# Performance work log

Hardware: AMD Instinct MI355X
Metric: run time of the kernel (lower is better)

Reference implementation:

```python
import jax, jax.numpy as jnp
import numpy as np

N_NODES = 100000


def _sage_conv(x, edge_index, W_l, W_r, b):
    # PyG SAGEConv (aggr='mean', root_weight=True, bias in lin_l):
    # out_i = W_l @ mean_{j in N(i)} x_j + b + W_r @ x_i
    src = edge_index[0]
    dst = edge_index[1]
    msg = x[src]                                              # [E, d] gather
    agg = jax.ops.segment_sum(msg, dst, num_segments=N_NODES)  # [N, d]
    deg = jax.ops.segment_sum(jnp.ones((src.shape[0],), x.dtype), dst,
                              num_segments=N_NODES)            # [N]
    agg = agg / jnp.maximum(deg, 1.0)[:, None]                 # mean, 0 if isolated
    return agg @ W_l.T + b + x @ W_r.T


def setup_inputs() -> dict:
    key = jax.random.key(0)
    ks = jax.random.split(key, 10)
    E, P = 1600000, 200000
    d_in, d_hid, d_out = 64, 128, 64
    s = 0.05
    return {
        "x": jax.random.normal(ks[0], (N_NODES, d_in), jnp.float32),
        "edge_index": jax.random.randint(ks[1], (2, E), 0, N_NODES, jnp.int32).astype(jnp.int64),
        "pairs": jax.random.randint(ks[2], (P, 2), 0, N_NODES, jnp.int32).astype(jnp.int64),
        "W1l": jax.random.normal(ks[3], (d_hid, d_in), jnp.float32) * s,
        "W1r": jax.random.normal(ks[4], (d_hid, d_in), jnp.float32) * s,
        "b1": jnp.zeros((d_hid,), jnp.float32),
        "W2l": jax.random.normal(ks[5], (d_out, d_hid), jnp.float32) * s,
        "W2r": jax.random.normal(ks[6], (d_out, d_hid), jnp.float32) * s,
        "b2": jnp.zeros((d_out,), jnp.float32),
        "Wlp": jax.random.normal(ks[7], (1, 2 * d_out), jnp.float32) * s,
        "blp": jnp.zeros((1,), jnp.float32),
    }


def reference(x, edge_index, pairs, W1l, W1r, b1, W2l, W2r, b2, Wlp, blp):
    h = _sage_conv(x, edge_index, W1l, W1r, b1)
    h = jax.nn.relu(h)
    h = _sage_conv(h, edge_index, W2l, W2r, b2)          # [N, d_out]
    src_emb = h[pairs[:, 0]]                              # [P, d_out]
    dst_emb = h[pairs[:, 1]]                              # [P, d_out]
    edge_emb = jnp.concatenate([src_emb, dst_emb], axis=1)  # [P, 2*d_out]
    logits = edge_emb @ Wlp.T + blp                       # [P, 1]
    return jax.nn.sigmoid(logits).squeeze(-1)             # [P]
```

## Files before the change

kernel.cpp:

```cpp
#include <hip/hip_runtime.h>


typedef __attribute__((ext_vector_type(8))) short bf16x8;
typedef __attribute__((ext_vector_type(4))) float f32x4;

#define NBLK_A 256

__device__ __forceinline__ unsigned short f2bf(float f) {
    unsigned u = __float_as_uint(f);
    u = u + 0x7fffu + ((u >> 16) & 1u);
    return (unsigned short)(u >> 16);
}
__device__ __forceinline__ float b2f(unsigned short s) {
    return __uint_as_float(((unsigned)s) << 16);
}
__device__ __forceinline__ float uflo(unsigned v) { return __uint_as_float(v << 16); }
__device__ __forceinline__ float ufhi(unsigned v) { return __uint_as_float(v & 0xffff0000u); }

__device__ __forceinline__ long load_idx(const void* p, long i, int is64) {
    if (is64) return (long)((const long long*)p)[i];
    return (long)((const int*)p)[i];
}

__device__ __forceinline__ int detect64_local(const void* p) {
    const unsigned* u = (const unsigned*)p;
    unsigned a = 0;
#pragma unroll
    for (int i = 0; i < 32; ++i) a |= u[2 * i + 1];
    return a == 0u;
}

__global__ void pre_kernel(const void* eidx, const float* __restrict__ x,
                           const float* __restrict__ W1l, const float* __restrict__ W1r,
                           const float* __restrict__ W2l, const float* __restrict__ W2r,
                           const float* __restrict__ b2, const float* __restrict__ Wlp,
                           const float* __restrict__ blp,
                           int* __restrict__ blk_hist, unsigned short* __restrict__ xa,
                           unsigned short* __restrict__ w1bf, float* __restrict__ wv,
                           int* __restrict__ flag,
                           long N, long E, int NBK, int chunk, int xcb) {
    int b = blockIdx.x;
    int tid = threadIdx.x;
    if (b < NBLK_A) {
        __shared__ int h[512];
        for (int i = tid; i < NBK; i += 256) h[i] = 0;
        __syncthreads();
        int is64 = detect64_local(eidx);
        long e0 = (long)b * chunk;
        long e1 = e0 + chunk; if (e1 > E) e1 = E;
        for (long e = e0 + tid; e < e1; e += 256) {
            long dst = load_idx(eidx, E + e, is64);
            atomicAdd(&h[(int)(dst >> 8)], 1);
        }
        __syncthreads();
        for (int i = tid; i < NBK; i += 256) blk_hist[i * NBLK_A + b] = h[i];
    } else if (b < NBLK_A + xcb) {
        long t = (long)(b - NBLK_A) * 256 + tid;
        long n = t >> 4;
        int q = (int)(t & 15);
        if (n >= N) return;
        float4 v = *(const float4*)&x[n * 64 + q * 4];
        uint2 u;
        u.x = (unsigned)f2bf(v.x) | ((unsigned)f2bf(v.y) << 16);
        u.y = (unsigned)f2bf(v.z) | ((unsigned)f2bf(v.w) << 16);
        *(uint2*)&xa[n * 128 + 64 + q * 4] = u;
    } else {
        if (tid == 0) *flag = detect64_local(eidx);
        if (tid < 128) {
            int k = tid;
            float s0 = 0.f, s1 = 0.f, s2 = 0.f, s3 = 0.f;
            for (int o = 0; o < 64; ++o) {
                float wl = Wlp[o], wr = Wlp[64 + o];
                float l = W2l[o * 128 + k], r = W2r[o * 128 + k];
                s0 += wl * l; s1 += wr * l; s2 += wl * r; s3 += wr * r;
            }
            wv[k] = s0; wv[128 + k] = s1; wv[256 + k] = s2; wv[384 + k] = s3;
            if (k == 0) {
                float c = blp[0];
                for (int o = 0; o < 64; ++o) c += (Wlp[o] + Wlp[64 + o]) * b2[o];
                wv[512] = c;
            }
        }
        for (int i = tid; i < 16384; i += 256) {
            int o = i >> 7, k = i & 127;
            float f = (k < 64) ? W1l[o * 64 + k] : W1r[o * 64 + (k - 64)];
            w1bf[i ^ ((o & 7) << 3)] = f2bf(f);
        }
    }
}

__global__ void bucket_total_kernel(const int* __restrict__ blk_hist, int* __restrict__ total) {
    __shared__ int ts[256];
    int k = blockIdx.x, t = threadIdx.x;
    ts[t] = blk_hist[k * NBLK_A + t];
    __syncthreads();
    for (int off = 128; off > 0; off >>= 1) {
        if (t < off) ts[t] += ts[t + off];
        __syncthreads();
    }
    if (t == 0) total[k] = ts[0];
}

__global__ void bucket_base_kernel(const int* __restrict__ total, int* __restrict__ base,
                                   int* __restrict__ row_start, int NBK, long N, long E) {
    int acc = 0;
    for (int k = 0; k < NBK; ++k) { base[k] = acc; acc += total[k]; }
    base[NBK] = acc;
    row_start[N] = (int)E;
}

__global__ void bucket_off_kernel(int* __restrict__ blk_hist, const int* __restrict__ base) {
    __shared__ int ts[256];
    int k = blockIdx.x, t = threadIdx.x;
    int v = blk_hist[k * NBLK_A + t];
    ts[t] = v; __syncthreads();
    for (int off = 1; off < 256; off <<= 1) {
        int u = (t >= off) ? ts[t - off] : 0;
        __syncthreads();
        ts[t] += u;
        __syncthreads();
    }
    blk_hist[k * NBLK_A + t] = base[k] + ts[t] - v;
}

__global__ void bucket_scatter_kernel(const void* eidx, const int* flag,
                                      const int* __restrict__ blk_hist,
                                      unsigned* __restrict__ ebuf, long E, int NBK, int chunk) {
    __shared__ int cur[512];
    int tid = threadIdx.x, b = blockIdx.x;
    for (int i = tid; i < NBK; i += 256) cur[i] = blk_hist[i * NBLK_A + b];
    __syncthreads();
    int is64 = *flag;
    long e0 = (long)b * chunk;
    long e1 = e0 + chunk; if (e1 > E) e1 = E;
    for (long e = e0 + tid; e < e1; e += 256) {
        long src = load_idx(eidx, e, is64);
        long dst = load_idx(eidx, E + e, is64);
        int pos = atomicAdd(&cur[(int)(dst >> 8)], 1);
        ebuf[pos] = (unsigned)src | ((unsigned)(dst & 255) << 24);
    }
}

__global__ void bucket_csr_kernel(const unsigned* __restrict__ ebuf, const int* __restrict__ base,
                                  int* __restrict__ csr_src, int* __restrict__ row_start, long N) {
    __shared__ int cnt[256], sc[256], cur[256];
    int k = blockIdx.x, t = threadIdx.x;
    int bstart = base[k], bend = base[k + 1];
    cnt[t] = 0;
    __syncthreads();
    for (int i = bstart + t; i < bend; i += 256)
        atomicAdd(&cnt[ebuf[i] >> 24], 1);
    __syncthreads();
    int c = cnt[t];
    sc[t] = c; __syncthreads();
    for (int off = 1; off < 256; off <<= 1) {
        int u = (t >= off) ? sc[t - off] : 0;
        __syncthreads();
        sc[t] += u;
        __syncthreads();
    }
    int loff = sc[t] - c;
    cur[t] = loff;
    long n = (long)k * 256 + t;
    if (n < N) row_start[n] = bstart + loff;
    __syncthreads();
    for (int i = bstart + t; i < bend; i += 256) {
        unsigned v = ebuf[i];
        int dl = (int)(v >> 24);
        int p = atomicAdd(&cur[dl], 1);
        csr_src[bstart + p] = (int)(v & 0xFFFFFFu);
    }
}

__global__ void gather_kernel(const int* __restrict__ rs, const int* __restrict__ csr,
                              const unsigned short* __restrict__ T,
                              unsigned short* __restrict__ Out, long N) {
    long gid = (long)blockIdx.x * 256 + threadIdx.x;
    long n = gid >> 6;
    if (n >= N) return;
    int lane = (int)(gid & 63);
    int lg = lane >> 4;
    int fq = lane & 15;
    int s = rs[n], e = rs[n + 1];
    unsigned boff = 64u + (unsigned)fq * 4u;
    float a0 = 0.f, a1 = 0.f, a2 = 0.f, a3 = 0.f;
    int j = s;
    for (; j + 16 <= e; j += 16) {
        unsigned o0 = ((unsigned)csr[j + lg] << 7) | boff;
        unsigned o1 = ((unsigned)csr[j + 4 + lg] << 7) | boff;
        unsigned o2 = ((unsigned)csr[j + 8 + lg] << 7) | boff;
        unsigned o3 = ((unsigned)csr[j + 12 + lg] << 7) | boff;
        uint2 r0 = *(const uint2*)&T[o0];
        uint2 r1 = *(const uint2*)&T[o1];
        uint2 r2 = *(const uint2*)&T[o2];
        uint2 r3 = *(const uint2*)&T[o3];
        a0 += uflo(r0.x); a1 += ufhi(r0.x); a2 += uflo(r0.y); a3 += ufhi(r0.y);
        a0 += uflo(r1.x); a1 += ufhi(r1.x); a2 += uflo(r1.y); a3 += ufhi(r1.y);
        a0 += uflo(r2.x); a1 += ufhi(r2.x); a2 += uflo(r2.y); a3 += ufhi(r2.y);
        a0 += uflo(r3.x); a1 += ufhi(r3.x); a2 += uflo(r3.y); a3 += ufhi(r3.y);
    }
    if (j < e) {
#pragma unroll
        for (int t = 0; t < 4; ++t) {
            int pos = j + 4 * t + lg;
            int ok = pos < e;
            unsigned oo = ((unsigned)csr[ok ? pos : s] << 7) | boff;
            uint2 r = *(const uint2*)&T[oo];
            float m = ok ? 1.f : 0.f;
            a0 += m * uflo(r.x); a1 += m * ufhi(r.x);
            a2 += m * uflo(r.y); a3 += m * ufhi(r.y);
        }
    }
    a0 += __shfl_xor(a0, 16, 64);  a1 += __shfl_xor(a1, 16, 64);
    a2 += __shfl_xor(a2, 16, 64);  a3 += __shfl_xor(a3, 16, 64);
    a0 += __shfl_xor(a0, 32, 64);  a1 += __shfl_xor(a1, 32, 64);
    a2 += __shfl_xor(a2, 32, 64);  a3 += __shfl_xor(a3, 32, 64);
    if (lg == 0) {
        float inv = 1.0f / fmaxf((float)(e - s), 1.0f);
        uint2 o;
        o.x = (unsigned)f2bf(a0 * inv) | ((unsigned)f2bf(a1 * inv) << 16);
        o.y = (unsigned)f2bf(a2 * inv) | ((unsigned)f2bf(a3 * inv) << 16);
        *(uint2*)&Out[((unsigned)n << 7) | ((unsigned)fq * 4u)] = o;
    }
}

__global__ __launch_bounds__(512) void fused_gemm_kernel(
        const unsigned short* __restrict__ A,
        const unsigned short* __restrict__ w1bf, const float* __restrict__ b1,
        const float* __restrict__ wv,
        float* __restrict__ ab, float* __restrict__ cd, long N) {
    __shared__ __align__(16) unsigned short wbuf[128 * 128];
    __shared__ __align__(16) unsigned short h1t[8][16 * 128];
    __shared__ float bs1[128];
    __shared__ float wvs[512];
    int tid = threadIdx.x;

    {
        const uint4* src = (const uint4*)w1bf;
        uint4* dst = (uint4*)wbuf;
#pragma unroll
        for (int i = 0; i < 4; ++i) dst[tid + i * 512] = src[tid + i * 512];
    }
    if (tid < 128) bs1[tid] = b1[tid];
    wvs[tid] = wv[tid];
    __syncthreads();

    int lane = tid & 63, wid = tid >> 6;
    int l16 = lane & 15, lg = lane >> 4;
    long n0 = (long)blockIdx.x * 128 + wid * 16;
    const unsigned short* A0 = A + (n0 + l16) * 128;
    unsigned short* hw = h1t[wid];

    f32x4 acc[8];
#pragma unroll
    for (int ot = 0; ot < 8; ++ot) acc[ot] = (f32x4){0.f, 0.f, 0.f, 0.f};

#pragma unroll
    for (int ks = 0; ks < 4; ++ks) {
        int k0 = ks * 32;
        bf16x8 a = *(const bf16x8*)&A0[k0 + 8 * lg];
#pragma unroll
        for (int ot = 0; ot < 8; ++ot) {
            int o = ot * 16 + l16;
            bf16x8 b = *(const bf16x8*)&wbuf[(o * 128 + k0 + 8 * lg) ^ ((o & 7) << 3)];
            acc[ot] = __builtin_amdgcn_mfma_f32_16x16x32_bf16(a, b, acc[ot], 0, 0, 0);
        }
    }
#pragma unroll
    for (int j = 0; j < 4; ++j) {
        int row = lg * 4 + j;
#pragma unroll
        for (int ot = 0; ot < 8; ++ot) {
            int col = ot * 16 + l16;
            float v = fmaxf(acc[ot][j] + bs1[col], 0.f);
            hw[(row * 128 + col) ^ ((row & 7) << 3)] = f2bf(v);
        }
    }
    __syncthreads();

    float da = 0.f, db = 0.f, dc = 0.f, dd = 0.f;
    int nl = l16;
#pragma unroll
    for (int t = 0; t < 4; ++t) {
        bf16x8 h = *(const bf16x8*)&hw[(nl * 128 + lg * 32 + t * 8) ^ ((nl & 7) << 3)];
#pragma unroll
        for (int e2 = 0; e2 < 8; ++e2) {
            float hv = b2f((unsigned short)h[e2]);
            int k = lg * 32 + t * 8 + e2;
            da += hv * wvs[k];       db += hv * wvs[128 + k];
            dc += hv * wvs[256 + k]; dd += hv * wvs[384 + k];
        }
    }
    da += __shfl_xor(da, 16, 64); db += __shfl_xor(db, 16, 64);
    dc += __shfl_xor(dc, 16, 64); dd += __shfl_xor(dd, 16, 64);
    da += __shfl_xor(da, 32, 64); db += __shfl_xor(db, 32, 64);
    dc += __shfl_xor(dc, 32, 64); dd += __shfl_xor(dd, 32, 64);
    long n = n0 + nl;
    if (lg == 0 && n < N) {
        *(float2*)&ab[n * 2] = make_float2(da, db);
        *(float2*)&cd[n * 2] = make_float2(dc, dd);
    }
}

__global__ void sgather_kernel(const int* __restrict__ rs, const int* __restrict__ csr,
                               const float* __restrict__ ab, const float* __restrict__ cd,
                               float* __restrict__ UV, long N) {
    long n = (long)blockIdx.x * 256 + threadIdx.x;
    if (n >= N) return;
    int s = rs[n], e = rs[n + 1];
    float sa = 0.f, sb = 0.f;
    int j = s;
    for (; j + 4 <= e; j += 4) {
        unsigned i0 = (unsigned)csr[j] * 2u, i1 = (unsigned)csr[j + 1] * 2u;
        unsigned i2 = (unsigned)csr[j + 2] * 2u, i3 = (unsigned)csr[j + 3] * 2u;
        float2 v0 = *(const float2*)&ab[i0];
        float2 v1 = *(const float2*)&ab[i1];
        float2 v2 = *(const float2*)&ab[i2];
        float2 v3 = *(const float2*)&ab[i3];
        sa += (v0.x + v1.x) + (v2.x + v3.x);
        sb += (v0.y + v1.y) + (v2.y + v3.y);
    }
    for (; j < e; ++j) {
        float2 v = *(const float2*)&ab[(unsigned)csr[j] * 2u];
        sa += v.x; sb += v.y;
    }
    float inv = 1.0f / fmaxf((float)(e - s), 1.0f);
    float2 cdv = *(const float2*)&cd[n * 2];
    *(float2*)&UV[n * 2] = make_float2(sa * inv + cdv.x, sb * inv + cdv.y);
}

__global__ void linkpred_kernel(const void* pairs, const int* flag,
                                const float* __restrict__ UV, const float* __restrict__ wv,
                                float* __restrict__ out, long P) {
    long p = (long)blockIdx.x * 256 + threadIdx.x;
    if (p >= P) return;
    int is64 = *flag;
    long s = load_idx(pairs, 2 * p, is64);
    long d = load_idx(pairs, 2 * p + 1, is64);
    float acc = UV[s * 2] + UV[d * 2 + 1] + wv[512];
    out[p] = 1.0f / (1.0f + expf(-acc));
}

extern "C" void kernel_launch(void* const* d_in, const int* in_sizes, int n_in,
                              void* d_out, int out_size, void* d_ws, size_t ws_size,
                              hipStream_t stream) {
    const float* x    = (const float*)d_in[0];
    const void*  eidx  = d_in[1];
    const void*  pairs = d_in[2];
    const float* W1l = (const float*)d_in[3];
    const float* W1r = (const float*)d_in[4];
    const float* b1  = (const float*)d_in[5];
    const float* W2l = (const float*)d_in[6];
    const float* W2r = (const float*)d_in[7];
    const float* b2  = (const float*)d_in[8];
    const float* Wlp = (const float*)d_in[9];
    const float* blp = (const float*)d_in[10];
    float* out = (float*)d_out;

    long N = in_sizes[0] / 64;
    long E = in_sizes[1] / 2;
    long P = in_sizes[2] / 2;
    long NP = (N + 127) & ~127L;
    int NBK = (int)((N + 255) >> 8);
    int chunk = (int)((E + NBLK_A - 1) / NBLK_A);
    int xcb = (int)((N * 16 + 255) / 256);

    char* w = (char*)d_ws;
    auto alloc = [&](size_t bytes) {
        char* p = w;
        w += (bytes + 255) & ~(size_t)255;
        return p;
    };
    int* row_start = (int*)alloc((N + 1) * sizeof(int));
    int* csr_src   = (int*)alloc(E * sizeof(int));
    int* blk_hist  = (int*)alloc((size_t)NBK * NBLK_A * sizeof(int));
    int* total     = (int*)alloc(NBK * sizeof(int));
    int* base      = (int*)alloc((NBK + 1) * sizeof(int));
    int* flag      = (int*)alloc(64);
    unsigned* ebuf = (unsigned*)alloc(E * sizeof(unsigned));
    unsigned short* xa   = (unsigned short*)alloc((size_t)NP * 128 * 2);
    unsigned short* w1bf = (unsigned short*)alloc(16384 * 2);
    float* ab = (float*)alloc((size_t)N * 2 * sizeof(float));
    float* cd = (float*)alloc((size_t)N * 2 * sizeof(float));
    float* UV = (float*)alloc((size_t)N * 2 * sizeof(float));
    float* wv = (float*)alloc(1024 * sizeof(float));

    unsigned pre_blocks = (unsigned)(NBLK_A + xcb + 1);
    pre_kernel<<<pre_blocks, 256, 0, stream>>>(eidx, x, W1l, W1r, W2l, W2r, b2, Wlp, blp,
                                               blk_hist, xa, w1bf, wv, flag,
                                               N, E, NBK, chunk, xcb);

    bucket_total_kernel<<<NBK, 256, 0, stream>>>(blk_hist, total);
    bucket_base_kernel<<<1, 1, 0, stream>>>(total, base, row_start, NBK, N, E);
    bucket_off_kernel<<<NBK, 256, 0, stream>>>(blk_hist, base);
    bucket_scatter_kernel<<<NBLK_A, 256, 0, stream>>>(eidx, flag, blk_hist, ebuf, E, NBK, chunk);
    bucket_csr_kernel<<<NBK, 256, 0, stream>>>(ebuf, base, csr_src, row_start, N);

    unsigned gth_blocks = (unsigned)((N * 64 + 255) / 256);
    gather_kernel<<<gth_blocks, 256, 0, stream>>>(row_start, csr_src, xa, xa, N);

    unsigned gblocks = (unsigned)(NP / 128);
    fused_gemm_kernel<<<gblocks, 512, 0, stream>>>(xa, w1bf, b1, wv, ab, cd, N);

    unsigned sgblocks = (unsigned)((N + 255) / 256);
    sgather_kernel<<<sgblocks, 256, 0, stream>>>(row_start, csr_src, ab, cd, UV, N);

    unsigned pblocks = (unsigned)((P + 255) / 256);
    linkpred_kernel<<<pblocks, 256, 0, stream>>>(pairs, flag, UV, wv, out, P);
}
```

Baseline: 151.5 us.

## Fuse neighbor gather into first-layer GEMM and merge bucket scan kernels

The first-layer mean aggregation moves into the GEMM kernel. Each wave gathers its 16 nodes into a swizzled LDS tile and feeds it straight to MFMA, so the aggregated bf16 features no longer round-trip through global memory. The x bf16 copy is compacted to 64 columns, and the layer-2 projection is now computed from the MFMA accumulators with shuffle reductions instead of going through an LDS h1 tile. The bucket-offset pipeline drops from three kernels to two: a per-bucket relative scan, then a parallel base scan, with base added inside scatter. The risk is lower parallelism in the gather, since one wave now handles 16 nodes one after another, and the launch bounds cap registers.

Result: faster. 148.3 us (-2.1%).

```diff
diff --git a/kernel.cpp b/kernel.cpp
--- a/kernel.cpp
+++ b/kernel.cpp
@@ -35,7 +35,7 @@
                            const float* __restrict__ W2l, const float* __restrict__ W2r,
                            const float* __restrict__ b2, const float* __restrict__ Wlp,
                            const float* __restrict__ blp,
-                           int* __restrict__ blk_hist, unsigned short* __restrict__ xa,
+                           int* __restrict__ blk_hist, unsigned short* __restrict__ xaown,
                            unsigned short* __restrict__ w1bf, float* __restrict__ wv,
                            int* __restrict__ flag,
                            long N, long E, int NBK, int chunk, int xcb) {
@@ -63,7 +63,7 @@
         uint2 u;
         u.x = (unsigned)f2bf(v.x) | ((unsigned)f2bf(v.y) << 16);
         u.y = (unsigned)f2bf(v.z) | ((unsigned)f2bf(v.w) << 16);
-        *(uint2*)&xa[n * 128 + 64 + q * 4] = u;
+        *(uint2*)&xaown[n * 64 + q * 4] = u;
     } else {
         if (tid == 0) *flag = detect64_local(eidx);
         if (tid < 128) {
@@ -89,27 +89,7 @@
     }
 }
 
-__global__ void bucket_total_kernel(const int* __restrict__ blk_hist, int* __restrict__ total) {
-    __shared__ int ts[256];
-    int k = blockIdx.x, t = threadIdx.x;
-    ts[t] = blk_hist[k * NBLK_A + t];
-    __syncthreads();
-    for (int off = 128; off > 0; off >>= 1) {
-        if (t < off) ts[t] += ts[t + off];
-        __syncthreads();
-    }
-    if (t == 0) total[k] = ts[0];
-}
-
-__global__ void bucket_base_kernel(const int* __restrict__ total, int* __restrict__ base,
-                                   int* __restrict__ row_start, int NBK, long N, long E) {
-    int acc = 0;
-    for (int k = 0; k < NBK; ++k) { base[k] = acc; acc += total[k]; }
-    base[NBK] = acc;
-    row_start[N] = (int)E;
-}
-
-__global__ void bucket_off_kernel(int* __restrict__ blk_hist, const int* __restrict__ base) {
+__global__ void bucket_relscan_kernel(int* __restrict__ blk_hist, int* __restrict__ total) {
     __shared__ int ts[256];
     int k = blockIdx.x, t = threadIdx.x;
     int v = blk_hist[k * NBLK_A + t];
@@ -120,15 +100,46 @@
         ts[t] += u;
         __syncthreads();
     }
-    blk_hist[k * NBLK_A + t] = base[k] + ts[t] - v;
+    blk_hist[k * NBLK_A + t] = ts[t] - v;
+    if (t == 255) total[k] = ts[255];
+}
+
+__global__ void base_kernel(const int* __restrict__ total, int* __restrict__ base,
+                            int* __restrict__ row_start, int NBK, long N, long E) {
+    __shared__ int ts[256];
+    int t = threadIdx.x;
+    int a = (t < NBK) ? total[t] : 0;
+    int b = (256 + t < NBK) ? total[256 + t] : 0;
+    ts[t] = a; __syncthreads();
+    for (int off = 1; off < 256; off <<= 1) {
+        int u = (t >= off) ? ts[t - off] : 0;
+        __syncthreads();
+        ts[t] += u;
+        __syncthreads();
+    }
+    int incl1 = ts[t];
+    int sum1 = ts[255];
+    if (t < NBK) base[t] = incl1 - a;
+    __syncthreads();
+    ts[t] = b; __syncthreads();
+    for (int off = 1; off < 256; off <<= 1) {
+        int u = (t >= off) ? ts[t - off] : 0;
+        __syncthreads();
+        ts[t] += u;
+        __syncthreads();
+    }
+    int incl2 = ts[t];
+    if (256 + t < NBK) base[256 + t] = sum1 + incl2 - b;
+    if (t == 255) base[NBK] = sum1 + incl2;
+    if (t == 0) row_start[N] = (int)E;
 }
 
 __global__ void bucket_scatter_kernel(const void* eidx, const int* flag,
-                                      const int* __restrict__ blk_hist,
+                                      const int* __restrict__ blk_hist, const int* __restrict__ base,
                                       unsigned* __restrict__ ebuf, long E, int NBK, int chunk) {
     __shared__ int cur[512];
     int tid = threadIdx.x, b = blockIdx.x;
-    for (int i = tid; i < NBK; i += 256) cur[i] = blk_hist[i * NBLK_A + b];
+    for (int i = tid; i < NBK; i += 256) cur[i] = blk_hist[i * NBLK_A + b] + base[i];
     __syncthreads();
     int is64 = *flag;
     long e0 = (long)b * chunk;
@@ -172,65 +183,14 @@
     }
 }
 
-__global__ void gather_kernel(const int* __restrict__ rs, const int* __restrict__ csr,
-                              const unsigned short* __restrict__ T,
-                              unsigned short* __restrict__ Out, long N) {
-    long gid = (long)blockIdx.x * 256 + threadIdx.x;
-    long n = gid >> 6;
-    if (n >= N) return;
-    int lane = (int)(gid & 63);
-    int lg = lane >> 4;
-    int fq = lane & 15;
-    int s = rs[n], e = rs[n + 1];
-    unsigned boff = 64u + (unsigned)fq * 4u;
-    float a0 = 0.f, a1 = 0.f, a2 = 0.f, a3 = 0.f;
-    int j = s;
-    for (; j + 16 <= e; j += 16) {
-        unsigned o0 = ((unsigned)csr[j + lg] << 7) | boff;
-        unsigned o1 = ((unsigned)csr[j + 4 + lg] << 7) | boff;
-        unsigned o2 = ((unsigned)csr[j + 8 + lg] << 7) | boff;
-        unsigned o3 = ((unsigned)csr[j + 12 + lg] << 7) | boff;
-        uint2 r0 = *(const uint2*)&T[o0];
-        uint2 r1 = *(const uint2*)&T[o1];
-        uint2 r2 = *(const uint2*)&T[o2];
-        uint2 r3 = *(const uint2*)&T[o3];
-        a0 += uflo(r0.x); a1 += ufhi(r0.x); a2 += uflo(r0.y); a3 += ufhi(r0.y);
-        a0 += uflo(r1.x); a1 += ufhi(r1.x); a2 += uflo(r1.y); a3 += ufhi(r1.y);
-        a0 += uflo(r2.x); a1 += ufhi(r2.x); a2 += uflo(r2.y); a3 += ufhi(r2.y);
-        a0 += uflo(r3.x); a1 += ufhi(r3.x); a2 += uflo(r3.y); a3 += ufhi(r3.y);
-    }
-    if (j < e) {
-#pragma unroll
-        for (int t = 0; t < 4; ++t) {
-            int pos = j + 4 * t + lg;
-            int ok = pos < e;
-            unsigned oo = ((unsigned)csr[ok ? pos : s] << 7) | boff;
-            uint2 r = *(const uint2*)&T[oo];
-            float m = ok ? 1.f : 0.f;
-            a0 += m * uflo(r.x); a1 += m * ufhi(r.x);
-            a2 += m * uflo(r.y); a3 += m * ufhi(r.y);
-        }
-    }
-    a0 += __shfl_xor(a0, 16, 64);  a1 += __shfl_xor(a1, 16, 64);
-    a2 += __shfl_xor(a2, 16, 64);  a3 += __shfl_xor(a3, 16, 64);
-    a0 += __shfl_xor(a0, 32, 64);  a1 += __shfl_xor(a1, 32, 64);
-    a2 += __shfl_xor(a2, 32, 64);  a3 += __shfl_xor(a3, 32, 64);
-    if (lg == 0) {
-        float inv = 1.0f / fmaxf((float)(e - s), 1.0f);
-        uint2 o;
-        o.x = (unsigned)f2bf(a0 * inv) | ((unsigned)f2bf(a1 * inv) << 16);
-        o.y = (unsigned)f2bf(a2 * inv) | ((unsigned)f2bf(a3 * inv) << 16);
-        *(uint2*)&Out[((unsigned)n << 7) | ((unsigned)fq * 4u)] = o;
-    }
-}
-
-__global__ __launch_bounds__(512) void fused_gemm_kernel(
-        const unsigned short* __restrict__ A,
+__global__ __launch_bounds__(512, 4) void fused_gg_kernel(
+        const int* __restrict__ rs, const int* __restrict__ csr,
+        const unsigned short* __restrict__ xaown,
         const unsigned short* __restrict__ w1bf, const float* __restrict__ b1,
         const float* __restrict__ wv,
         float* __restrict__ ab, float* __restrict__ cd, long N) {
     __shared__ __align__(16) unsigned short wbuf[128 * 128];
-    __shared__ __align__(16) unsigned short h1t[8][16 * 128];
+    __shared__ __align__(16) unsigned short aggt[8][16 * 64];
     __shared__ float bs1[128];
     __shared__ float wvs[512];
     int tid = threadIdx.x;
@@ -243,22 +203,70 @@
     }
     if (tid < 128) bs1[tid] = b1[tid];
     wvs[tid] = wv[tid];
-    __syncthreads();
 
     int lane = tid & 63, wid = tid >> 6;
     int l16 = lane & 15, lg = lane >> 4;
     long n0 = (long)blockIdx.x * 128 + wid * 16;
-    const unsigned short* A0 = A + (n0 + l16) * 128;
-    unsigned short* hw = h1t[wid];
+    unsigned short* agg = aggt[wid];
+    unsigned boff = (unsigned)l16 * 4u;
+
+    for (int nl = 0; nl < 16; ++nl) {
+        long n = n0 + nl;
+        int s = 0, e = 0;
+        if (n < N) { s = rs[n]; e = rs[n + 1]; }
+        float a0 = 0.f, a1 = 0.f, a2 = 0.f, a3 = 0.f;
+        int j = s;
+        for (; j + 16 <= e; j += 16) {
+            unsigned o0 = ((unsigned)csr[j + lg] << 6) | boff;
+            unsigned o1 = ((unsigned)csr[j + 4 + lg] << 6) | boff;
+            unsigned o2 = ((unsigned)csr[j + 8 + lg] << 6) | boff;
+            unsigned o3 = ((unsigned)csr[j + 12 + lg] << 6) | boff;
+            uint2 r0 = *(const uint2*)&xaown[o0];
+            uint2 r1 = *(const uint2*)&xaown[o1];
+            uint2 r2 = *(const uint2*)&xaown[o2];
+            uint2 r3 = *(const uint2*)&xaown[o3];
+            a0 += uflo(r0.x); a1 += ufhi(r0.x); a2 += uflo(r0.y); a3 += ufhi(r0.y);
+            a0 += uflo(r1.x); a1 += ufhi(r1.x); a2 += uflo(r1.y); a3 += ufhi(r1.y);
+            a0 += uflo(r2.x); a1 += ufhi(r2.x); a2 += uflo(r2.y); a3 += ufhi(r2.y);
+            a0 += uflo(r3.x); a1 += ufhi(r3.x); a2 += uflo(r3.y); a3 += ufhi(r3.y);
+        }
+        if (j < e) {
+#pragma unroll
+            for (int t = 0; t < 4; ++t) {
+                int pos = j + 4 * t + lg;
+                int ok = pos < e;
+                unsigned oo = ((unsigned)csr[ok ? pos : s] << 6) | boff;
+                uint2 r = *(const uint2*)&xaown[oo];
+                float m = ok ? 1.f : 0.f;
+                a0 += m * uflo(r.x); a1 += m * ufhi(r.x);
+                a2 += m * uflo(r.y); a3 += m * ufhi(r.y);
+            }
+        }
+        a0 += __shfl_xor(a0, 16, 64);  a1 += __shfl_xor(a1, 16, 64);
+        a2 += __shfl_xor(a2, 16, 64);  a3 += __shfl_xor(a3, 16, 64);
+        a0 += __shfl_xor(a0, 32, 64);  a1 += __shfl_xor(a1, 32, 64);
+        a2 += __shfl_xor(a2, 32, 64);  a3 += __shfl_xor(a3, 32, 64);
+        if (lg == 0) {
+            float inv = 1.0f / fmaxf((float)(e - s), 1.0f);
+            uint2 o;
+            o.x = (unsigned)f2bf(a0 * inv) | ((unsigned)f2bf(a1 * inv) << 16);
+            o.y = (unsigned)f2bf(a2 * inv) | ((unsigned)f2bf(a3 * inv) << 16);
+            int eo = (l16 * 4) ^ ((nl & 7) << 3);
+            *(uint2*)&agg[nl * 64 + eo] = o;
+        }
+    }
+    __syncthreads();
 
     f32x4 acc[8];
 #pragma unroll
     for (int ot = 0; ot < 8; ++ot) acc[ot] = (f32x4){0.f, 0.f, 0.f, 0.f};
-
+    const unsigned short* A0 = xaown + (n0 + l16) * 64;
 #pragma unroll
     for (int ks = 0; ks < 4; ++ks) {
         int k0 = ks * 32;
-        bf16x8 a = *(const bf16x8*)&A0[k0 + 8 * lg];
+        bf16x8 a;
+        if (ks < 2) a = *(const bf16x8*)&agg[l16 * 64 + ((k0 + 8 * lg) ^ ((l16 & 7) << 3))];
+        else        a = *(const bf16x8*)&A0[(k0 - 64) + 8 * lg];
 #pragma unroll
         for (int ot = 0; ot < 8; ++ot) {
             int o = ot * 16 + l16;
@@ -266,39 +274,30 @@
             acc[ot] = __builtin_amdgcn_mfma_f32_16x16x32_bf16(a, b, acc[ot], 0, 0, 0);
         }
     }
+
 #pragma unroll
     for (int j = 0; j < 4; ++j) {
-        int row = lg * 4 + j;
+        float da = 0.f, db = 0.f, dc = 0.f, dd = 0.f;
 #pragma unroll
         for (int ot = 0; ot < 8; ++ot) {
             int col = ot * 16 + l16;
-            float v = fmaxf(acc[ot][j] + bs1[col], 0.f);
-            hw[(row * 128 + col) ^ ((row & 7) << 3)] = f2bf(v);
-        }
-    }
-    __syncthreads();
-
-    float da = 0.f, db = 0.f, dc = 0.f, dd = 0.f;
-    int nl = l16;
-#pragma unroll
-    for (int t = 0; t < 4; ++t) {
-        bf16x8 h = *(const bf16x8*)&hw[(nl * 128 + lg * 32 + t * 8) ^ ((nl & 7) << 3)];
-#pragma unroll
-        for (int e2 = 0; e2 < 8; ++e2) {
-            float hv = b2f((unsigned short)h[e2]);
-            int k = lg * 32 + t * 8 + e2;
-            da += hv * wvs[k];       db += hv * wvs[128 + k];
-            dc += hv * wvs[256 + k]; dd += hv * wvs[384 + k];
-        }
-    }
-    da += __shfl_xor(da, 16, 64); db += __shfl_xor(db, 16, 64);
-    dc += __shfl_xor(dc, 16, 64); dd += __shfl_xor(dd, 16, 64);
-    da += __shfl_xor(da, 32, 64); db += __shfl_xor(db, 32, 64);
-    dc += __shfl_xor(dc, 32, 64); dd += __shfl_xor(dd, 32, 64);
-    long n = n0 + nl;
-    if (lg == 0 && n < N) {
-        *(float2*)&ab[n * 2] = make_float2(da, db);
-        *(float2*)&cd[n * 2] = make_float2(dc, dd);
+            float hv = fmaxf(acc[ot][j] + bs1[col], 0.f);
+            da += hv * wvs[col];       db += hv * wvs[128 + col];
+            dc += hv * wvs[256 + col]; dd += hv * wvs[384 + col];
+        }
+        da += __shfl_xor(da, 1, 64); db += __shfl_xor(db, 1, 64);
+        dc += __shfl_xor(dc, 1, 64); dd += __shfl_xor(dd, 1, 64);
+        da += __shfl_xor(da, 2, 64); db += __shfl_xor(db, 2, 64);
+        dc += __shfl_xor(dc, 2, 64); dd += __shfl_xor(dd, 2, 64);
+        da += __shfl_xor(da, 4, 64); db += __shfl_xor(db, 4, 64);
+        dc += __shfl_xor(dc, 4, 64); dd += __shfl_xor(dd, 4, 64);
+        da += __shfl_xor(da, 8, 64); db += __shfl_xor(db, 8, 64);
+        dc += __shfl_xor(dc, 8, 64); dd += __shfl_xor(dd, 8, 64);
+        long n = n0 + lg * 4 + j;
+        if (l16 == 0 && n < N) {
+            *(float2*)&ab[n * 2] = make_float2(da, db);
+            *(float2*)&cd[n * 2] = make_float2(dc, dd);
+        }
     }
 }
 
@@ -378,8 +377,8 @@
     int* base      = (int*)alloc((NBK + 1) * sizeof(int));
     int* flag      = (int*)alloc(64);
     unsigned* ebuf = (unsigned*)alloc(E * sizeof(unsigned));
-    unsigned short* xa   = (unsigned short*)alloc((size_t)NP * 128 * 2);
-    unsigned short* w1bf = (unsigned short*)alloc(16384 * 2);
+    unsigned short* xaown = (unsigned short*)alloc((size_t)NP * 64 * 2);
+    unsigned short* w1bf  = (unsigned short*)alloc(16384 * 2);
     float* ab = (float*)alloc((size_t)N * 2 * sizeof(float));
     float* cd = (float*)alloc((size_t)N * 2 * sizeof(float));
     float* UV = (float*)alloc((size_t)N * 2 * sizeof(float));
@@ -387,20 +386,16 @@
 
     unsigned pre_blocks = (unsigned)(NBLK_A + xcb + 1);
     pre_kernel<<<pre_blocks, 256, 0, stream>>>(eidx, x, W1l, W1r, W2l, W2r, b2, Wlp, blp,
-                                               blk_hist, xa, w1bf, wv, flag,
+                                               blk_hist, xaown, w1bf, wv, flag,
                                                N, E, NBK, chunk, xcb);
 
-    bucket_total_kernel<<<NBK, 256, 0, stream>>>(blk_hist, total);
-    bucket_base_kernel<<<1, 1, 0, stream>>>(total, base, row_start, NBK, N, E);
-    bucket_off_kernel<<<NBK, 256, 0, stream>>>(blk_hist, base);
-    bucket_scatter_kernel<<<NBLK_A, 256, 0, stream>>>(eidx, flag, blk_hist, ebuf, E, NBK, chunk);
+    bucket_relscan_kernel<<<NBK, 256, 0, stream>>>(blk_hist, total);
+    base_kernel<<<1, 256, 0, stream>>>(total, base, row_start, NBK, N, E);
+    bucket_scatter_kernel<<<NBLK_A, 256, 0, stream>>>(eidx, flag, blk_hist, base, ebuf, E, NBK, chunk);
     bucket_csr_kernel<<<NBK, 256, 0, stream>>>(ebuf, base, csr_src, row_start, N);
 
-    unsigned gth_blocks = (unsigned)((N * 64 + 255) / 256);
-    gather_kernel<<<gth_blocks, 256, 0, stream>>>(row_start, csr_src, xa, xa, N);
-
     unsigned gblocks = (unsigned)(NP / 128);
-    fused_gemm_kernel<<<gblocks, 512, 0, stream>>>(xa, w1bf, b1, wv, ab, cd, N);
+    fused_gg_kernel<<<gblocks, 512, 0, stream>>>(row_start, csr_src, xaown, w1bf, b1, wv, ab, cd, N);
 
     unsigned sgblocks = (unsigned)((N + 255) / 256);
     sgather_kernel<<<sgblocks, 256, 0, stream>>>(row_start, csr_src, ab, cd, UV, N);
```
